# Kernel tuning notes

Hardware: AMD Instinct MI355X
Metric: run time of the kernel (lower is better)

The kernel has to match this reference:

```python
import jax, jax.numpy as jnp
import numpy as np

N = 50000          # nodes
E = 600000         # edges
IN, H, HID = 3, 128, 64   # input_size, embed_size, decoder hidden
L = 5              # block_number (GRU layers)
EPS = 1e-12


def _l2norm(v):
    # F.normalize(v, p=2, dim=1)
    return v / jnp.maximum(jnp.linalg.norm(v, axis=1, keepdims=True), EPS)


def setup_inputs() -> dict:
    key = jax.random.key(0)
    ks = jax.random.split(key, 12)
    s = 0.05
    x = jax.random.normal(ks[0], (N, IN), dtype=jnp.float32)
    edge_idx = jax.random.randint(ks[1], (2, E), 0, N, dtype=jnp.int64)
    return {
        "x": x,
        "edge_idx": edge_idx,
        # encoder embed: Linear(IN, H)
        "W_embed": jax.random.normal(ks[2], (H, IN), dtype=jnp.float32) * s,
        "b_embed": jnp.zeros((H,), dtype=jnp.float32),
        # L stacked GRU(H, H) params, torch gate order (r, z, n)
        "w_ih": jax.random.normal(ks[3], (L, 3 * H, H), dtype=jnp.float32) * s,
        "w_hh": jax.random.normal(ks[4], (L, 3 * H, H), dtype=jnp.float32) * s,
        "b_ih": jax.random.normal(ks[5], (L, 3 * H), dtype=jnp.float32) * s,
        "b_hh": jax.random.normal(ks[6], (L, 3 * H), dtype=jnp.float32) * s,
        # decoder: Linear(H, HID) -> ReLU -> Linear(HID, 1)
        "W_hid": jax.random.normal(ks[7], (HID, H), dtype=jnp.float32) * s,
        "b_hid": jnp.zeros((HID,), dtype=jnp.float32),
        "W_out": jax.random.normal(ks[8], (1, HID), dtype=jnp.float32) * s,
        "b_out": jnp.zeros((1,), dtype=jnp.float32),
    }


def reference(x, edge_idx, W_embed, b_embed, w_ih, w_hh, b_ih, b_hh,
              W_hid, b_hid, W_out, b_out):
    row, col = edge_idx[0], edge_idx[1]
    n = x.shape[0]

    # symmetric degree normalization (deg + 1)^-0.5, identical every layer
    deg = jnp.zeros((n,), dtype=x.dtype).at[col].add(1.0) + 1.0
    dinv = deg ** -0.5
    norm = dinv[row] * dinv[col]            # [E]

    h0 = _l2norm(jax.nn.relu(x @ W_embed.T + b_embed))  # [N, H]

    def step(h, params):
        wih, whh, bih, bhh = params
        # message + add-aggregate: out[col] += norm * h[row]
        msg = norm[:, None] * h[row]                     # [E, H]
        agg = jax.ops.segment_sum(msg, col, num_segments=n)  # [N, H]
        # GRU step: input = agg, hidden = h (torch gate order r, z, n)
        gi = agg @ wih.T + bih                           # [N, 3H]
        gh = h @ whh.T + bhh                             # [N, 3H]
        i_r, i_z, i_n = jnp.split(gi, 3, axis=1)
        h_r, h_z, h_n = jnp.split(gh, 3, axis=1)
        r = jax.nn.sigmoid(i_r + h_r)
        zg = jax.nn.sigmoid(i_z + h_z)
        ng = jnp.tanh(i_n + r * h_n)
        hn = _l2norm((1.0 - zg) * ng + zg * h)
        return hn, hn

    _, hs = jax.lax.scan(step, h0, (w_ih, w_hh, b_ih, b_hh))  # hs: [L, N, H]
    all_h = jnp.concatenate([h0[None], hs], axis=0)           # [L+1, N, H]
    z = jnp.max(all_h, axis=0)                                # layer-wise max-pool

    z = jax.nn.relu(z @ W_hid.T + b_hid)
    return z @ W_out.T + b_out                                # [N, 1]
```

## Files before the change

kernel.cpp:

```cpp
#include <hip/hip_runtime.h>
#include <math.h>


#define NTHREADS 256
#define SCAN_CHUNK 1024

typedef __attribute__((ext_vector_type(8))) short s16x8;
typedef __attribute__((ext_vector_type(4))) float f32x4;

union U8 { s16x8 v; ushort4 h[2]; int4 q; };

__device__ __forceinline__ unsigned short f2bf(float f) {
  union { float f; unsigned u; } x; x.f = f;
  unsigned u = x.u + 0x7FFFu + ((x.u >> 16) & 1u);
  return (unsigned short)(u >> 16);
}
__device__ __forceinline__ float bf2f(unsigned short s) {
  union { unsigned u; float f; } x; x.u = ((unsigned)s) << 16;
  return x.f;
}


__global__ void count_deg(const int* __restrict__ col, int* deg, int E) {
  int e = blockIdx.x * NTHREADS + threadIdx.x;
  if (e < E) atomicAdd(&deg[col[e]], 1);
}

__global__ void block_reduce(const int* __restrict__ cnt, int* __restrict__ bsum,
                             float* __restrict__ dinv, int n) {
  __shared__ int red[NTHREADS];
  int b = blockIdx.x, t = threadIdx.x;
  int base = b * SCAN_CHUNK + t * 4;
  int s = 0;
#pragma unroll
  for (int i = 0; i < 4; ++i) {
    int idx = base + i;
    if (idx < n) {
      int c = cnt[idx];
      s += c;
      dinv[idx] = rsqrtf((float)c + 1.0f);
    }
  }
  red[t] = s;
  __syncthreads();
  for (int off = NTHREADS / 2; off > 0; off >>= 1) {
    if (t < off) red[t] += red[t + off];
    __syncthreads();
  }
  if (t == 0) bsum[b] = red[0];
}

__global__ void scan_partials(const int* __restrict__ bsum, int* __restrict__ boff,
                              int* __restrict__ row_ptr_n, int nb) {
  int t = threadIdx.x;
  int s = (t < nb) ? bsum[t] : 0;
  int orig = s;
#pragma unroll
  for (int off = 1; off < 64; off <<= 1) {
    int v = __shfl_up(s, off);
    if (t >= off) s += v;
  }
  if (t < nb) boff[t] = s - orig;
  if (t == nb - 1) *row_ptr_n = s;
}

__global__ void scan_final(const int* __restrict__ cnt, const int* __restrict__ boff,
                           int* __restrict__ row_ptr, int* __restrict__ cursor, int n) {
  __shared__ int sums[NTHREADS];
  int b = blockIdx.x, t = threadIdx.x;
  int base = b * SCAN_CHUNK + t * 4;
  int v[4];
  int s = 0;
#pragma unroll
  for (int i = 0; i < 4; ++i) { int idx = base + i; v[i] = (idx < n) ? cnt[idx] : 0; s += v[i]; }
  sums[t] = s;
  __syncthreads();
  for (int off = 1; off < NTHREADS; off <<= 1) {
    int a = (t >= off) ? sums[t - off] : 0;
    __syncthreads();
    sums[t] += a;
    __syncthreads();
  }
  int run = boff[b] + sums[t] - s;
#pragma unroll
  for (int i = 0; i < 4; ++i) {
    int idx = base + i;
    if (idx < n) { row_ptr[idx] = run; cursor[idx] = run; }
    run += v[i];
  }
}

__global__ void scatter_edges(const int* __restrict__ row, const int* __restrict__ col,
                              int* cursor, int* __restrict__ src, int E) {
  int e = blockIdx.x * NTHREADS + threadIdx.x;
  if (e >= E) return;
  int r = row[e], c = col[e];
  int p = atomicAdd(&cursor[c], 1);
  src[p] = r;
}


__global__ void pack_weights(const float* __restrict__ w_ih, const float* __restrict__ w_hh,
                             unsigned short* __restrict__ out) {
  int idx = blockIdx.x * NTHREADS + threadIdx.x;
  if (idx >= 491520) return;
  int e = idx & 7;
  int lane = (idx >> 3) & 63;
  int ft = (idx >> 9) & 7;
  int v = idx >> 12;
  int g = v % 6;
  int u = v / 6;
  int ks = u & 3;
  int layer = u >> 2;
  int k = 32 * ks + (e & 3) + 4 * ((lane >> 4) & 3) + 16 * (e >> 2);
  int j = 16 * ft + (lane & 15);
  const float* src = (g < 3) ? w_ih : w_hh;
  int gate = g % 3;
  float val = src[(size_t)layer * 49152 + (size_t)(gate * 128 + j) * 128 + k];
  out[idx] = f2bf(val);
}

__global__ void pack_whid(const float* __restrict__ W_hid, unsigned short* __restrict__ out) {
  int idx = blockIdx.x * NTHREADS + threadIdx.x;
  if (idx >= 8192) return;
  int e = idx & 7;
  int lane = (idx >> 3) & 63;
  int ft = (idx >> 9) & 3;
  int ks = idx >> 11;
  int k = 32 * ks + (e & 3) + 4 * ((lane >> 4) & 3) + 16 * (e >> 2);
  int j = 16 * ft + (lane & 15);
  out[idx] = f2bf(W_hid[j * 128 + k]);
}


__global__ void encoder(const float* __restrict__ x, const float* __restrict__ W,
                        const float* __restrict__ b, unsigned short* __restrict__ hb, int n) {
  int node = blockIdx.x * 4 + (threadIdx.x >> 6);
  int lane = threadIdx.x & 63;
  if (node >= n) return;
  float x0 = x[node * 3 + 0], x1 = x[node * 3 + 1], x2 = x[node * 3 + 2];
  int j0 = lane, j1 = lane + 64;
  float v0 = fmaxf(fmaf(W[j0 * 3 + 2], x2, fmaf(W[j0 * 3 + 1], x1, fmaf(W[j0 * 3], x0, b[j0]))), 0.f);
  float v1 = fmaxf(fmaf(W[j1 * 3 + 2], x2, fmaf(W[j1 * 3 + 1], x1, fmaf(W[j1 * 3], x0, b[j1]))), 0.f);
  float ss = v0 * v0 + v1 * v1;
#pragma unroll
  for (int sh = 32; sh > 0; sh >>= 1) ss += __shfl_down(ss, sh);
  ss = __shfl(ss, 0);
  float sc = 1.0f / fmaxf(sqrtf(ss), 1e-12f);
  size_t base = (size_t)node * 128;
  hb[base + j0] = f2bf(v0 * sc);
  hb[base + j1] = f2bf(v1 * sc);
}


__global__ void aggregate(const int* __restrict__ row_ptr, const int* __restrict__ src,
                          const float* __restrict__ dinv, const unsigned short* __restrict__ hb,
                          unsigned short* __restrict__ aggb, int n) {
  int node = blockIdx.x * 4 + (threadIdx.x >> 6);
  int lane = threadIdx.x & 63;
  if (node >= n) return;
  const unsigned* hw = (const unsigned*)hb;
  int pb = row_ptr[node], pe = row_ptr[node + 1];
  float aL[4] = {0.f, 0.f, 0.f, 0.f};
  float aH[4] = {0.f, 0.f, 0.f, 0.f};
  int p = pb;
  for (; p + 8 <= pe; p += 8) {
    int s[8]; unsigned u[8]; float w[8];
#pragma unroll
    for (int i = 0; i < 8; ++i) s[i] = src[p + i];
#pragma unroll
    for (int i = 0; i < 8; ++i) {
      w[i] = dinv[s[i]];
      u[i] = hw[(size_t)s[i] * 64 + lane];
    }
#pragma unroll
    for (int i = 0; i < 8; ++i) {
      aL[i & 3] = fmaf(w[i], bf2f((unsigned short)(u[i] & 0xFFFFu)), aL[i & 3]);
      aH[i & 3] = fmaf(w[i], bf2f((unsigned short)(u[i] >> 16)), aH[i & 3]);
    }
  }
  if (p + 4 <= pe) {
    int s[4]; unsigned u[4]; float w[4];
#pragma unroll
    for (int i = 0; i < 4; ++i) s[i] = src[p + i];
#pragma unroll
    for (int i = 0; i < 4; ++i) {
      w[i] = dinv[s[i]];
      u[i] = hw[(size_t)s[i] * 64 + lane];
    }
#pragma unroll
    for (int i = 0; i < 4; ++i) {
      aL[i] = fmaf(w[i], bf2f((unsigned short)(u[i] & 0xFFFFu)), aL[i]);
      aH[i] = fmaf(w[i], bf2f((unsigned short)(u[i] >> 16)), aH[i]);
    }
    p += 4;
  }
  for (; p < pe; ++p) {
    int s = src[p];
    float w = dinv[s];
    unsigned u = hw[(size_t)s * 64 + lane];
    aL[0] = fmaf(w, bf2f((unsigned short)(u & 0xFFFFu)), aL[0]);
    aH[0] = fmaf(w, bf2f((unsigned short)(u >> 16)), aH[0]);
  }
  float dc = dinv[node];
  float a0 = ((aL[0] + aL[1]) + (aL[2] + aL[3])) * dc;
  float a1 = ((aH[0] + aH[1]) + (aH[2] + aH[3])) * dc;
  unsigned o = ((unsigned)f2bf(a1) << 16) | (unsigned)f2bf(a0);
  ((unsigned*)(aggb + (size_t)node * 128))[lane] = o;
}


__global__ __launch_bounds__(1024) void gru_mfma(
    const unsigned short* __restrict__ aggb, const unsigned short* __restrict__ hbc,
    unsigned short* __restrict__ hbn,
    const int4* __restrict__ wpk, const float* __restrict__ bih,
    const float* __restrict__ bhh, int n) {
  __shared__ unsigned short aggS[64 * 132];
  __shared__ unsigned short hS[64 * 132];
  __shared__ float partS[64 * 8];
  __shared__ float scv[64];
  int tid = threadIdx.x;
  int base = blockIdx.x * 64;
  int w = tid >> 6, l = tid & 63;
  int mh = w & 1, fh = w >> 1;
  int lr = l & 15, lg = l >> 4;
  int jj = fh * 16 + lr;

#pragma unroll
  for (int rep = 0; rep < 2; ++rep) {
    int idx = tid + rep * 1024;
    int row = idx >> 5, c4 = idx & 31;
    int gr = base + row; if (gr > n - 1) gr = n - 1;
    ushort4 ua = *(const ushort4*)(aggb + (size_t)gr * 128 + c4 * 4);
    ushort4 uh = *(const ushort4*)(hbc + (size_t)gr * 128 + c4 * 4);
    *(ushort4*)&aggS[row * 132 + c4 * 4] = ua;
    *(ushort4*)&hS[row * 132 + c4 * 4] = uh;
  }
  __syncthreads();

  f32x4 acc[2][6];
#pragma unroll
  for (int mt = 0; mt < 2; ++mt)
#pragma unroll
    for (int g = 0; g < 6; ++g) { acc[mt][g][0] = 0.f; acc[mt][g][1] = 0.f; acc[mt][g][2] = 0.f; acc[mt][g][3] = 0.f; }

#pragma unroll
  for (int ks = 0; ks < 4; ++ks) {
    U8 fa[2], fhh[2];
#pragma unroll
    for (int mt = 0; mt < 2; ++mt) {
      int boff = (mh * 32 + mt * 16 + lr) * 132 + ks * 32 + lg * 4;
      fa[mt].h[0] = *(const ushort4*)&aggS[boff];
      fa[mt].h[1] = *(const ushort4*)&aggS[boff + 16];
      fhh[mt].h[0] = *(const ushort4*)&hS[boff];
      fhh[mt].h[1] = *(const ushort4*)&hS[boff + 16];
    }
#pragma unroll
    for (int g = 0; g < 6; ++g) {
      U8 bw; bw.q = wpk[((ks * 6 + g) * 8 + fh) * 64 + l];
      const U8& a0 = (g < 3) ? fa[0] : fhh[0];
      const U8& a1 = (g < 3) ? fa[1] : fhh[1];
      acc[0][g] = __builtin_amdgcn_mfma_f32_16x16x32_bf16(a0.v, bw.v, acc[0][g], 0, 0, 0);
      acc[1][g] = __builtin_amdgcn_mfma_f32_16x16x32_bf16(a1.v, bw.v, acc[1][g], 0, 0, 0);
    }
  }

  float br = bih[jj], bz = bih[128 + jj], bn = bih[256 + jj];
  float cr = bhh[jj], cz = bhh[128 + jj], cn = bhh[256 + jj];
  float hn_out[2][4];
#pragma unroll
  for (int mt = 0; mt < 2; ++mt)
#pragma unroll
    for (int e = 0; e < 4; ++e) {
      int row = mh * 32 + mt * 16 + lg * 4 + e;
      float ir = acc[mt][0][e], iz = acc[mt][1][e], inn = acc[mt][2][e];
      float hr = acc[mt][3][e], hz = acc[mt][4][e], hnv = acc[mt][5][e];
      float r = 1.f / (1.f + __expf(-(ir + hr + br + cr)));
      float z = 1.f / (1.f + __expf(-(iz + hz + bz + cz)));
      float ng = tanhf(inn + bn + r * (hnv + cn));
      float hv = bf2f(hS[row * 132 + jj]);
      float hn = (1.f - z) * ng + z * hv;
      hn_out[mt][e] = hn;
      float p = hn * hn;
      p += __shfl_xor(p, 1);
      p += __shfl_xor(p, 2);
      p += __shfl_xor(p, 4);
      p += __shfl_xor(p, 8);
      if (lr == 0) partS[row * 8 + fh] = p;
    }
  __syncthreads();
  if (tid < 64) {
    float ss = 0.f;
#pragma unroll
    for (int f = 0; f < 8; ++f) ss += partS[tid * 8 + f];
    scv[tid] = 1.f / fmaxf(sqrtf(ss), 1e-12f);
  }
  __syncthreads();

#pragma unroll
  for (int mt = 0; mt < 2; ++mt)
#pragma unroll
    for (int e = 0; e < 4; ++e) {
      int row = mh * 32 + mt * 16 + lg * 4 + e;
      aggS[row * 132 + jj] = f2bf(hn_out[mt][e] * scv[row]);
    }
  __syncthreads();

#pragma unroll
  for (int rep = 0; rep < 2; ++rep) {
    int idx = tid + rep * 1024;
    int row = idx >> 5, c4 = idx & 31;
    int gr = base + row;
    if (gr < n) {
      ushort4 hv4 = *(const ushort4*)&aggS[row * 132 + c4 * 4];
      *(ushort4*)(hbn + (size_t)gr * 128 + c4 * 4) = hv4;
    }
  }
}


__global__ __launch_bounds__(256) void decoder_mfma(
    const unsigned short* __restrict__ h0, const unsigned short* __restrict__ h1,
    const unsigned short* __restrict__ h2, const unsigned short* __restrict__ h3,
    const unsigned short* __restrict__ h4, const unsigned short* __restrict__ h5,
    const int4* __restrict__ wdpk, const float* __restrict__ bh,
    const float* __restrict__ Wo, const float* __restrict__ bo,
    float* __restrict__ out, int n) {
  __shared__ unsigned short zS[64 * 132];
  int tid = threadIdx.x;
  int base = blockIdx.x * 64;
  const unsigned short* hp[6] = {h0, h1, h2, h3, h4, h5};
#pragma unroll
  for (int rep = 0; rep < 8; ++rep) {
    int idx = tid + rep * 256;
    int row = idx >> 5, c4 = idx & 31;
    int gr = base + row; if (gr > n - 1) gr = n - 1;
    size_t o = (size_t)gr * 128 + c4 * 4;
    ushort4 uu[6];
#pragma unroll
    for (int li = 0; li < 6; ++li) uu[li] = *(const ushort4*)(hp[li] + o);
    ushort4 m = uu[0];
#pragma unroll
    for (int li = 1; li < 6; ++li) {
      m.x = (bf2f(uu[li].x) > bf2f(m.x)) ? uu[li].x : m.x;
      m.y = (bf2f(uu[li].y) > bf2f(m.y)) ? uu[li].y : m.y;
      m.z = (bf2f(uu[li].z) > bf2f(m.z)) ? uu[li].z : m.z;
      m.w = (bf2f(uu[li].w) > bf2f(m.w)) ? uu[li].w : m.w;
    }
    *(ushort4*)&zS[row * 132 + c4 * 4] = m;
  }
  __syncthreads();
  int w = tid >> 6, l = tid & 63;
  int lr = l & 15, lg = l >> 4;
  f32x4 acc[4];
#pragma unroll
  for (int ft = 0; ft < 4; ++ft) { acc[ft][0] = 0.f; acc[ft][1] = 0.f; acc[ft][2] = 0.f; acc[ft][3] = 0.f; }
#pragma unroll
  for (int ks = 0; ks < 4; ++ks) {
    U8 fz;
    int boff = (w * 16 + lr) * 132 + ks * 32 + lg * 4;
    fz.h[0] = *(const ushort4*)&zS[boff];
    fz.h[1] = *(const ushort4*)&zS[boff + 16];
#pragma unroll
    for (int ft = 0; ft < 4; ++ft) {
      U8 bw; bw.q = wdpk[(ks * 4 + ft) * 64 + l];
      acc[ft] = __builtin_amdgcn_mfma_f32_16x16x32_bf16(fz.v, bw.v, acc[ft], 0, 0, 0);
    }
  }
  float s[4] = {0.f, 0.f, 0.f, 0.f};
#pragma unroll
  for (int ft = 0; ft < 4; ++ft) {
    int j = ft * 16 + lr;
    float bj = bh[j], wj = Wo[j];
#pragma unroll
    for (int e = 0; e < 4; ++e) {
      float hid = fmaxf(acc[ft][e] + bj, 0.f);
      s[e] = fmaf(hid, wj, s[e]);
    }
  }
#pragma unroll
  for (int e = 0; e < 4; ++e) {
    float v = s[e];
    v += __shfl_xor(v, 1);
    v += __shfl_xor(v, 2);
    v += __shfl_xor(v, 4);
    v += __shfl_xor(v, 8);
    if (lr == 0) {
      int gr = base + w * 16 + lg * 4 + e;
      if (gr < n) out[gr] = v + bo[0];
    }
  }
}


extern "C" void kernel_launch(void* const* d_in, const int* in_sizes, int n_in,
                              void* d_out, int out_size, void* d_ws, size_t ws_size,
                              hipStream_t stream) {
  const float* x       = (const float*)d_in[0];
  const int*   edge    = (const int*)d_in[1];
  const float* W_embed = (const float*)d_in[2];
  const float* b_embed = (const float*)d_in[3];
  const float* w_ih    = (const float*)d_in[4];
  const float* w_hh    = (const float*)d_in[5];
  const float* b_ih    = (const float*)d_in[6];
  const float* b_hh    = (const float*)d_in[7];
  const float* W_hid   = (const float*)d_in[8];
  const float* b_hid   = (const float*)d_in[9];
  const float* W_out   = (const float*)d_in[10];
  const float* b_out   = (const float*)d_in[11];
  float* out = (float*)d_out;

  const int N = in_sizes[0] / 3;
  const int E = in_sizes[1] / 2;
  const int NB = (N + SCAN_CHUNK - 1) / SCAN_CHUNK;

  char* ws = (char*)d_ws;
  size_t off = 0;
  auto alloc = [&](size_t bytes) -> void* {
    void* p = ws + off;
    off = (off + bytes + 511) & ~(size_t)511;
    return p;
  };
  int*   deg     = (int*)alloc((size_t)N * 4);
  float* dinv    = (float*)alloc((size_t)N * 4);
  int*   row_ptr = (int*)alloc((size_t)(N + 1) * 4);
  int*   cursor  = (int*)alloc((size_t)N * 4);
  int*   bsum    = (int*)alloc((size_t)NB * 4);
  int*   boff    = (int*)alloc((size_t)NB * 4);
  int*   srcv    = (int*)alloc((size_t)E * 4);
  unsigned short* wpack  = (unsigned short*)alloc((size_t)491520 * 2);
  unsigned short* wdpack = (unsigned short*)alloc((size_t)8192 * 2);
  unsigned short* aggb   = (unsigned short*)alloc((size_t)N * 128 * 2);
  unsigned short* hbs[6];
  for (int i = 0; i < 6; ++i) hbs[i] = (unsigned short*)alloc((size_t)N * 128 * 2);

  const int* erow = edge;
  const int* ecol = edge + E;

  hipMemsetAsync(deg, 0, (size_t)N * 4, stream);
  count_deg<<<(E + NTHREADS - 1) / NTHREADS, NTHREADS, 0, stream>>>(ecol, deg, E);
  block_reduce<<<NB, NTHREADS, 0, stream>>>(deg, bsum, dinv, N);
  scan_partials<<<1, 64, 0, stream>>>(bsum, boff, row_ptr + N, NB);
  scan_final<<<NB, NTHREADS, 0, stream>>>(deg, boff, row_ptr, cursor, N);
  scatter_edges<<<(E + NTHREADS - 1) / NTHREADS, NTHREADS, 0, stream>>>(erow, ecol, cursor, srcv, E);

  pack_weights<<<(491520 + NTHREADS - 1) / NTHREADS, NTHREADS, 0, stream>>>(w_ih, w_hh, wpack);
  pack_whid<<<32, NTHREADS, 0, stream>>>(W_hid, wdpack);

  encoder<<<(N + 3) / 4, NTHREADS, 0, stream>>>(x, W_embed, b_embed, hbs[0], N);

  for (int l = 0; l < 5; ++l) {
    aggregate<<<(N + 3) / 4, NTHREADS, 0, stream>>>(row_ptr, srcv, dinv, hbs[l], aggb, N);
    gru_mfma<<<(N + 63) / 64, 1024, 0, stream>>>(
        aggb, hbs[l], hbs[l + 1],
        (const int4*)(wpack + (size_t)l * 98304),
        b_ih + (size_t)l * 384, b_hh + (size_t)l * 384, N);
  }

  decoder_mfma<<<(N + 63) / 64, NTHREADS, 0, stream>>>(
      hbs[0], hbs[1], hbs[2], hbs[3], hbs[4], hbs[5],
      (const int4*)wdpack, b_hid, W_out, b_out, out, N);
}
```

Before: 430.0 us.

## Pre-scale node features by inverse sqrt degree to drop per-edge dinv gather

```diff
diff --git a/kernel.cpp b/kernel.cpp
--- a/kernel.cpp
+++ b/kernel.cpp
@@ -27,7 +27,7 @@
 }
 
 __global__ void block_reduce(const int* __restrict__ cnt, int* __restrict__ bsum,
-                             float* __restrict__ dinv, int n) {
+                             float* __restrict__ dinv, float* __restrict__ rdinv, int n) {
   __shared__ int red[NTHREADS];
   int b = blockIdx.x, t = threadIdx.x;
   int base = b * SCAN_CHUNK + t * 4;
@@ -39,6 +39,7 @@
       int c = cnt[idx];
       s += c;
       dinv[idx] = rsqrtf((float)c + 1.0f);
+      rdinv[idx] = sqrtf((float)c + 1.0f);
     }
   }
   red[t] = s;
@@ -134,7 +135,8 @@
 
 
 __global__ void encoder(const float* __restrict__ x, const float* __restrict__ W,
-                        const float* __restrict__ b, unsigned short* __restrict__ hb, int n) {
+                        const float* __restrict__ b, const float* __restrict__ dinv,
+                        unsigned short* __restrict__ hd, int n) {
   int node = blockIdx.x * 4 + (threadIdx.x >> 6);
   int lane = threadIdx.x & 63;
   if (node >= n) return;
@@ -147,60 +149,38 @@
   for (int sh = 32; sh > 0; sh >>= 1) ss += __shfl_down(ss, sh);
   ss = __shfl(ss, 0);
   float sc = 1.0f / fmaxf(sqrtf(ss), 1e-12f);
+  float dv = dinv[node];
   size_t base = (size_t)node * 128;
-  hb[base + j0] = f2bf(v0 * sc);
-  hb[base + j1] = f2bf(v1 * sc);
+  hd[base + j0] = f2bf(v0 * sc * dv);
+  hd[base + j1] = f2bf(v1 * sc * dv);
 }
 
 
 __global__ void aggregate(const int* __restrict__ row_ptr, const int* __restrict__ src,
-                          const float* __restrict__ dinv, const unsigned short* __restrict__ hb,
+                          const float* __restrict__ dinv, const unsigned short* __restrict__ hd,
                           unsigned short* __restrict__ aggb, int n) {
   int node = blockIdx.x * 4 + (threadIdx.x >> 6);
   int lane = threadIdx.x & 63;
   if (node >= n) return;
-  const unsigned* hw = (const unsigned*)hb;
+  const unsigned* hw = (const unsigned*)hd;
   int pb = row_ptr[node], pe = row_ptr[node + 1];
   float aL[4] = {0.f, 0.f, 0.f, 0.f};
   float aH[4] = {0.f, 0.f, 0.f, 0.f};
-  int p = pb;
-  for (; p + 8 <= pe; p += 8) {
-    int s[8]; unsigned u[8]; float w[8];
-#pragma unroll
-    for (int i = 0; i < 8; ++i) s[i] = src[p + i];
+  for (int p = pb; p < pe; p += 8) {
+    unsigned u[8]; float wv[8];
 #pragma unroll
     for (int i = 0; i < 8; ++i) {
-      w[i] = dinv[s[i]];
-      u[i] = hw[(size_t)s[i] * 64 + lane];
+      int q = p + i;
+      int ok = q < pe;
+      int s = src[ok ? q : pb];
+      wv[i] = ok ? 1.f : 0.f;
+      u[i] = hw[(size_t)s * 64 + lane];
     }
 #pragma unroll
     for (int i = 0; i < 8; ++i) {
-      aL[i & 3] = fmaf(w[i], bf2f((unsigned short)(u[i] & 0xFFFFu)), aL[i & 3]);
-      aH[i & 3] = fmaf(w[i], bf2f((unsigned short)(u[i] >> 16)), aH[i & 3]);
-    }
-  }
-  if (p + 4 <= pe) {
-    int s[4]; unsigned u[4]; float w[4];
-#pragma unroll
-    for (int i = 0; i < 4; ++i) s[i] = src[p + i];
-#pragma unroll
-    for (int i = 0; i < 4; ++i) {
-      w[i] = dinv[s[i]];
-      u[i] = hw[(size_t)s[i] * 64 + lane];
-    }
-#pragma unroll
-    for (int i = 0; i < 4; ++i) {
-      aL[i] = fmaf(w[i], bf2f((unsigned short)(u[i] & 0xFFFFu)), aL[i]);
-      aH[i] = fmaf(w[i], bf2f((unsigned short)(u[i] >> 16)), aH[i]);
-    }
-    p += 4;
-  }
-  for (; p < pe; ++p) {
-    int s = src[p];
-    float w = dinv[s];
-    unsigned u = hw[(size_t)s * 64 + lane];
-    aL[0] = fmaf(w, bf2f((unsigned short)(u & 0xFFFFu)), aL[0]);
-    aH[0] = fmaf(w, bf2f((unsigned short)(u >> 16)), aH[0]);
+      aL[i & 3] = fmaf(wv[i], bf2f((unsigned short)(u[i] & 0xFFFFu)), aL[i & 3]);
+      aH[i & 3] = fmaf(wv[i], bf2f((unsigned short)(u[i] >> 16)), aH[i & 3]);
+    }
   }
   float dc = dinv[node];
   float a0 = ((aL[0] + aL[1]) + (aL[2] + aL[3])) * dc;
@@ -211,14 +191,16 @@
 
 
 __global__ __launch_bounds__(1024) void gru_mfma(
-    const unsigned short* __restrict__ aggb, const unsigned short* __restrict__ hbc,
-    unsigned short* __restrict__ hbn,
+    const unsigned short* __restrict__ aggb, const unsigned short* __restrict__ hdc,
+    unsigned short* __restrict__ hdn, const float* __restrict__ dinv,
+    const float* __restrict__ rdinv,
     const int4* __restrict__ wpk, const float* __restrict__ bih,
     const float* __restrict__ bhh, int n) {
   __shared__ unsigned short aggS[64 * 132];
   __shared__ unsigned short hS[64 * 132];
   __shared__ float partS[64 * 8];
   __shared__ float scv[64];
+  __shared__ float dS[64], rS[64];
   int tid = threadIdx.x;
   int base = blockIdx.x * 64;
   int w = tid >> 6, l = tid & 63;
@@ -226,13 +208,18 @@
   int lr = l & 15, lg = l >> 4;
   int jj = fh * 16 + lr;
 
+  if (tid < 64) {
+    int gr = base + tid; if (gr > n - 1) gr = n - 1;
+    dS[tid] = dinv[gr];
+    rS[tid] = rdinv[gr];
+  }
 #pragma unroll
   for (int rep = 0; rep < 2; ++rep) {
     int idx = tid + rep * 1024;
     int row = idx >> 5, c4 = idx & 31;
     int gr = base + row; if (gr > n - 1) gr = n - 1;
     ushort4 ua = *(const ushort4*)(aggb + (size_t)gr * 128 + c4 * 4);
-    ushort4 uh = *(const ushort4*)(hbc + (size_t)gr * 128 + c4 * 4);
+    ushort4 uh = *(const ushort4*)(hdc + (size_t)gr * 128 + c4 * 4);
     *(ushort4*)&aggS[row * 132 + c4 * 4] = ua;
     *(ushort4*)&hS[row * 132 + c4 * 4] = uh;
   }
@@ -273,12 +260,13 @@
 #pragma unroll
     for (int e = 0; e < 4; ++e) {
       int row = mh * 32 + mt * 16 + lg * 4 + e;
+      float rr = rS[row];
       float ir = acc[mt][0][e], iz = acc[mt][1][e], inn = acc[mt][2][e];
-      float hr = acc[mt][3][e], hz = acc[mt][4][e], hnv = acc[mt][5][e];
+      float hr = acc[mt][3][e] * rr, hz = acc[mt][4][e] * rr, hnv = acc[mt][5][e] * rr;
       float r = 1.f / (1.f + __expf(-(ir + hr + br + cr)));
       float z = 1.f / (1.f + __expf(-(iz + hz + bz + cz)));
       float ng = tanhf(inn + bn + r * (hnv + cn));
-      float hv = bf2f(hS[row * 132 + jj]);
+      float hv = bf2f(hS[row * 132 + jj]) * rr;
       float hn = (1.f - z) * ng + z * hv;
       hn_out[mt][e] = hn;
       float p = hn * hn;
@@ -302,7 +290,7 @@
 #pragma unroll
     for (int e = 0; e < 4; ++e) {
       int row = mh * 32 + mt * 16 + lg * 4 + e;
-      aggS[row * 132 + jj] = f2bf(hn_out[mt][e] * scv[row]);
+      aggS[row * 132 + jj] = f2bf(hn_out[mt][e] * scv[row] * dS[row]);
     }
   __syncthreads();
 
@@ -313,7 +301,7 @@
     int gr = base + row;
     if (gr < n) {
       ushort4 hv4 = *(const ushort4*)&aggS[row * 132 + c4 * 4];
-      *(ushort4*)(hbn + (size_t)gr * 128 + c4 * 4) = hv4;
+      *(ushort4*)(hdn + (size_t)gr * 128 + c4 * 4) = hv4;
     }
   }
 }
@@ -323,6 +311,7 @@
     const unsigned short* __restrict__ h0, const unsigned short* __restrict__ h1,
     const unsigned short* __restrict__ h2, const unsigned short* __restrict__ h3,
     const unsigned short* __restrict__ h4, const unsigned short* __restrict__ h5,
+    const float* __restrict__ rdinv,
     const int4* __restrict__ wdpk, const float* __restrict__ bh,
     const float* __restrict__ Wo, const float* __restrict__ bo,
     float* __restrict__ out, int n) {
@@ -367,6 +356,13 @@
       acc[ft] = __builtin_amdgcn_mfma_f32_16x16x32_bf16(fz.v, bw.v, acc[ft], 0, 0, 0);
     }
   }
+  int rowb = base + w * 16 + lg * 4;
+  float rr[4];
+#pragma unroll
+  for (int e = 0; e < 4; ++e) {
+    int gr = rowb + e; if (gr > n - 1) gr = n - 1;
+    rr[e] = rdinv[gr];
+  }
   float s[4] = {0.f, 0.f, 0.f, 0.f};
 #pragma unroll
   for (int ft = 0; ft < 4; ++ft) {
@@ -374,7 +370,7 @@
     float bj = bh[j], wj = Wo[j];
 #pragma unroll
     for (int e = 0; e < 4; ++e) {
-      float hid = fmaxf(acc[ft][e] + bj, 0.f);
+      float hid = fmaxf(fmaf(acc[ft][e], rr[e], bj), 0.f);
       s[e] = fmaf(hid, wj, s[e]);
     }
   }
@@ -386,7 +382,7 @@
     v += __shfl_xor(v, 4);
     v += __shfl_xor(v, 8);
     if (lr == 0) {
-      int gr = base + w * 16 + lg * 4 + e;
+      int gr = rowb + e;
       if (gr < n) out[gr] = v + bo[0];
     }
   }
@@ -423,11 +419,12 @@
   };
   int*   deg     = (int*)alloc((size_t)N * 4);
   float* dinv    = (float*)alloc((size_t)N * 4);
+  float* rdinv   = (float*)alloc((size_t)N * 4);
   int*   row_ptr = (int*)alloc((size_t)(N + 1) * 4);
   int*   cursor  = (int*)alloc((size_t)N * 4);
   int*   bsum    = (int*)alloc((size_t)NB * 4);
   int*   boff    = (int*)alloc((size_t)NB * 4);
-  int*   srcv    = (int*)alloc((size_t)E * 4);
+  int*   srcv    = (int*)alloc((size_t)(E + 8) * 4);
   unsigned short* wpack  = (unsigned short*)alloc((size_t)491520 * 2);
   unsigned short* wdpack = (unsigned short*)alloc((size_t)8192 * 2);
   unsigned short* aggb   = (unsigned short*)alloc((size_t)N * 128 * 2);
@@ -439,7 +436,7 @@
 
   hipMemsetAsync(deg, 0, (size_t)N * 4, stream);
   count_deg<<<(E + NTHREADS - 1) / NTHREADS, NTHREADS, 0, stream>>>(ecol, deg, E);
-  block_reduce<<<NB, NTHREADS, 0, stream>>>(deg, bsum, dinv, N);
+  block_reduce<<<NB, NTHREADS, 0, stream>>>(deg, bsum, dinv, rdinv, N);
   scan_partials<<<1, 64, 0, stream>>>(bsum, boff, row_ptr + N, NB);
   scan_final<<<NB, NTHREADS, 0, stream>>>(deg, boff, row_ptr, cursor, N);
   scatter_edges<<<(E + NTHREADS - 1) / NTHREADS, NTHREADS, 0, stream>>>(erow, ecol, cursor, srcv, E);
@@ -447,17 +444,17 @@
   pack_weights<<<(491520 + NTHREADS - 1) / NTHREADS, NTHREADS, 0, stream>>>(w_ih, w_hh, wpack);
   pack_whid<<<32, NTHREADS, 0, stream>>>(W_hid, wdpack);
 
-  encoder<<<(N + 3) / 4, NTHREADS, 0, stream>>>(x, W_embed, b_embed, hbs[0], N);
+  encoder<<<(N + 3) / 4, NTHREADS, 0, stream>>>(x, W_embed, b_embed, dinv, hbs[0], N);
 
   for (int l = 0; l < 5; ++l) {
     aggregate<<<(N + 3) / 4, NTHREADS, 0, stream>>>(row_ptr, srcv, dinv, hbs[l], aggb, N);
     gru_mfma<<<(N + 63) / 64, 1024, 0, stream>>>(
-        aggb, hbs[l], hbs[l + 1],
+        aggb, hbs[l], hbs[l + 1], dinv, rdinv,
         (const int4*)(wpack + (size_t)l * 98304),
         b_ih + (size_t)l * 384, b_hh + (size_t)l * 384, N);
   }
 
   decoder_mfma<<<(N + 63) / 64, NTHREADS, 0, stream>>>(
-      hbs[0], hbs[1], hbs[2], hbs[3], hbs[4], hbs[5],
+      hbs[0], hbs[1], hbs[2], hbs[3], hbs[4], hbs[5], rdinv,
       (const int4*)wdpack, b_hid, W_out, b_out, out, N);
 }
```

Measured after the change: 414.4 us. 1.04x faster.
